# Optimization experiments

Measured on AMD Instinct MI355X. Metric: run time of the kernel, lower is better.

The kernel has to match this reference:

```python
import jax, jax.numpy as jnp
import numpy as np

EMBD_DIM = 512
HIDDEN_DIM = 512
TARGET_DIM = 128
BATCH = 64
MAX_SET = 2048


def setup_inputs() -> dict:
    key = jax.random.key(0)
    ks = jax.random.split(key, 10)
    E, H, T = EMBD_DIM, HIDDEN_DIM, TARGET_DIM
    s = lambda fan_in: 1.0 / np.sqrt(fan_in)
    return {
        "words": jax.random.normal(ks[0], (BATCH, MAX_SET, E), dtype=jnp.float32),
        # attention_layer: Linear(2E -> H) followed by tanh; v: (H, 1)
        "W_att": jax.random.uniform(ks[1], (2 * E, H), jnp.float32, -s(2 * E), s(2 * E)),
        "b_att": jax.random.uniform(ks[2], (H,), jnp.float32, -s(2 * E), s(2 * E)),
        "v": jax.random.normal(ks[3], (H, 1), dtype=jnp.float32),
        # pred_net: Linear(E,H) -> ReLU -> Linear(H,H) -> ReLU -> Linear(H,T)
        "W1": jax.random.uniform(ks[4], (E, H), jnp.float32, -s(E), s(E)),
        "b1": jax.random.uniform(ks[5], (H,), jnp.float32, -s(E), s(E)),
        "W2": jax.random.uniform(ks[6], (H, H), jnp.float32, -s(H), s(H)),
        "b2": jax.random.uniform(ks[7], (H,), jnp.float32, -s(H), s(H)),
        "W3": jax.random.uniform(ks[8], (H, T), jnp.float32, -s(H), s(H)),
        "b3": jax.random.uniform(ks[9], (T,), jnp.float32, -s(H), s(H)),
    }


def reference(words, W_att, b_att, v, W1, b1, W2, b2, W3, b3):
    # words: [B, S, E]. A row is "valid" iff its feature-sum is nonzero
    # (matches words.sum(2).abs().sign() in the torch code).
    mask = jnp.sign(jnp.abs(words.sum(-1)))           # [B, S], 0/1 float
    lengths = mask.sum(axis=1, keepdims=True)          # [B, 1]
    # context = mean over valid rows (padded rows are exactly zero)
    context = words.sum(axis=1, keepdims=True) / lengths[..., None]  # [B, 1, E]
    context = jnp.broadcast_to(context, words.shape)   # [B, S, E]

    x = jnp.concatenate([words, context], axis=-1)     # [B, S, 2E]
    h = jnp.tanh(x @ W_att + b_att)                    # [B, S, H]
    scores = (h @ v)[..., 0]                           # [B, S]

    # per-segment softmax over valid rows only (masked_select + per-batch
    # Softmax in the original == masked softmax here)
    scores = jnp.where(mask > 0, scores, jnp.full_like(scores, -1e30))
    attn = jax.nn.softmax(scores, axis=1)              # [B, S]

    rep = jnp.einsum("bs,bse->be", attn, words)        # [B, E]

    pred = jax.nn.relu(rep @ W1 + b1)
    pred = jax.nn.relu(pred @ W2 + b2)
    pred = pred @ W3 + b3                              # [B, T]
    return pred
```

## Files before the change

### kernel.cpp

```cpp
#include <hip/hip_runtime.h>
#include <hip/hip_bf16.h>
#include <hip/hip_fp16.h>
#include <math.h>

#define B 64
#define S 2048
#define E 512
#define HD 512
#define TD 128
#define M_TOT (B*S)

#define OFF_MASK   0
#define OFF_CTXP   (OFF_MASK + B*S)
#define OFF_LENP   (OFF_CTXP + 8*B*E)
#define OFF_CB     (OFF_LENP + 8*B)
#define OFF_REPP   (OFF_CB + B*HD)
#define OFF_SCP    (OFF_REPP + 8*B*E)
#define OFF_WPK    (OFF_SCP + 2*B*S)
#define OFF_WH     (OFF_WPK + 131072)
#define WS_NEED_FLOATS ((size_t)OFF_WH + (size_t)B*S*E/2)

typedef __attribute__((ext_vector_type(8))) short short8;
typedef __attribute__((ext_vector_type(4))) float f32x4;
typedef __attribute__((ext_vector_type(4))) unsigned short ushort4_t;

__device__ inline unsigned int f2hu(float x) {
    __half h = __float2half(x);
    unsigned short u; __builtin_memcpy(&u, &h, 2); return (unsigned int)u;
}
__device__ inline float hu2f(unsigned short u) {
    __half h; __builtin_memcpy(&h, &u, 2); return __half2float(h);
}

__device__ inline float fast_tanh(float x) {
    float a = fabsf(x);
    float e = __expf(-2.0f * a);
    float r = (1.0f - e) / (1.0f + e);
    return copysignf(r, x);
}

__global__ __launch_bounds__(256)
void k0_pack(const float* __restrict__ W_att, unsigned short* __restrict__ Wpk)
{
    int tid = blockIdx.x*256 + threadIdx.x;
    int e = tid >> 9, h = tid & 511;
    float w = W_att[(size_t)e*HD + h];
    int kstep = e >> 5, kb = (e >> 3) & 3, j = e & 7, f = h >> 4, l15 = h & 15;
    size_t dst = ((((size_t)kstep*32 + f)*64) + kb*16 + l15)*8 + j;
    Wpk[dst] = (unsigned short)f2hu(w);
}

template<bool WRITE_H>
__global__ __launch_bounds__(256)
void k1_maskcol(const float* __restrict__ words, float* __restrict__ mask,
                float* __restrict__ ctxp, float* __restrict__ lenp,
                unsigned short* __restrict__ wordsH)
{
    int bid = blockIdx.x;
    int b = bid >> 3, ch = bid & 7;
    int t = threadIdx.x;
    int w = t >> 6, l = t & 63;
    __shared__ __align__(16) float colred[4][E];
    __shared__ float lenred[4];
    const float* base = words + (size_t)(b * S + ch * 256) * E;
    unsigned short* hbase = wordsH + (size_t)(b * S + ch * 256) * E;
    float4 c0 = make_float4(0.f,0.f,0.f,0.f), c1 = make_float4(0.f,0.f,0.f,0.f);
    float wlen = 0.0f;
    for (int r = w; r < 256; r += 4) {
        const float* row = base + (size_t)r * E;
        float4 a  = *(const float4*)(row + 4*l);
        float4 bb = *(const float4*)(row + 256 + 4*l);
        if (WRITE_H) {
            ushort4_t ha, hb;
            ha[0]=(unsigned short)f2hu(a.x);  ha[1]=(unsigned short)f2hu(a.y);
            ha[2]=(unsigned short)f2hu(a.z);  ha[3]=(unsigned short)f2hu(a.w);
            hb[0]=(unsigned short)f2hu(bb.x); hb[1]=(unsigned short)f2hu(bb.y);
            hb[2]=(unsigned short)f2hu(bb.z); hb[3]=(unsigned short)f2hu(bb.w);
            *(ushort4_t*)(hbase + (size_t)r*E + 4*l)       = ha;
            *(ushort4_t*)(hbase + (size_t)r*E + 256 + 4*l) = hb;
        }
        float rs = a.x+a.y+a.z+a.w + bb.x+bb.y+bb.z+bb.w;
        #pragma unroll
        for (int m = 1; m < 64; m <<= 1) rs += __shfl_xor(rs, m);
        c0.x += a.x;  c0.y += a.y;  c0.z += a.z;  c0.w += a.w;
        c1.x += bb.x; c1.y += bb.y; c1.z += bb.z; c1.w += bb.w;
        if (l == 0) {
            float mv = (rs != 0.0f) ? 1.0f : 0.0f;
            mask[(size_t)b*S + ch*256 + r] = mv;
            wlen += mv;
        }
    }
    *(float4*)&colred[w][4*l]       = c0;
    *(float4*)&colred[w][256 + 4*l] = c1;
    if (l == 0) lenred[w] = wlen;
    __syncthreads();
    float s1 = colred[0][t]+colred[1][t]+colred[2][t]+colred[3][t];
    float s2 = colred[0][t+256]+colred[1][t+256]+colred[2][t+256]+colred[3][t+256];
    size_t o = ((size_t)ch * B + b) * E;
    ctxp[o + t]       = s1;
    ctxp[o + t + 256] = s2;
    if (t == 0) lenp[ch*B + b] = lenred[0]+lenred[1]+lenred[2]+lenred[3];
}

__global__ __launch_bounds__(256)
void k2_cb(const float* __restrict__ W_att, const float* __restrict__ b_att,
           const float* __restrict__ ctxp, const float* __restrict__ lenp,
           float* __restrict__ cb)
{
    int bid = blockIdx.x;
    int b = bid >> 1, hc = bid & 1;
    int t = threadIdx.x;
    __shared__ float ctxL[E];
    float len = 0.f;
    #pragma unroll
    for (int k = 0; k < 8; ++k) len += lenp[k*B + b];
    float inv = 1.0f / len;
    for (int c = t; c < E; c += 256) {
        float sv = 0.f;
        #pragma unroll
        for (int k = 0; k < 8; ++k) sv += ctxp[((size_t)k*B + b)*E + c];
        ctxL[c] = sv * inv;
    }
    __syncthreads();
    int h = hc*256 + t;
    const float* Wb = W_att + (size_t)E * HD;
    float a0 = b_att[h], a1 = 0.f, a2 = 0.f, a3 = 0.f;
    #pragma unroll 4
    for (int e = 0; e < E; e += 4) {
        a0 += ctxL[e]   * Wb[(size_t)e*HD + h];
        a1 += ctxL[e+1] * Wb[(size_t)(e+1)*HD + h];
        a2 += ctxL[e+2] * Wb[(size_t)(e+2)*HD + h];
        a3 += ctxL[e+3] * Wb[(size_t)(e+3)*HD + h];
    }
    cb[(size_t)b*HD + h] = (a0 + a1) + (a2 + a3);
}

template<bool F16>
__global__ __launch_bounds__(512, 4)
void k3_scores(const float* __restrict__ words,
               const unsigned short* __restrict__ wordsH,
               const unsigned short* __restrict__ Wpk,
               const float* __restrict__ cb, const float* __restrict__ v,
               float* __restrict__ scp)
{
    __shared__ __align__(16) unsigned char smem[16384];
    int bid = blockIdx.x;
    int mt = bid >> 1, nc = bid & 1;
    int m0 = mt * 128;
    int b  = m0 >> 11;
    int t = threadIdx.x;
    int lane = t & 63, wid = t >> 6;
    int wr = wid >> 2, wc = wid & 3;

    f32x4 acc[4][4];
    #pragma unroll
    for (int i = 0; i < 4; ++i)
        #pragma unroll
        for (int j = 0; j < 4; ++j) acc[i][j] = (f32x4)0.0f;

    int r = t >> 2, kq = t & 3;
    const float* aSrcF = words + (size_t)(m0 + r)*E + kq*8;
    const unsigned short* aSrcH = wordsH + (size_t)(m0 + r)*E + kq*8;
    int abase = (r >> 4)*1024 + kq*256 + (r & 15)*16;

    float4 pF[2];
    uint4  pH;

    auto LOADA = [&](int ks) {
        if constexpr (F16) {
            pH = *(const uint4*)(aSrcH + ks*32);
        } else {
            const float* _s = aSrcF + ks*32;
            pF[0] = *(const float4*)(_s); pF[1] = *(const float4*)(_s+4);
        }
    };
    auto STAGEA = [&](unsigned char* buf) {
        if constexpr (F16) {
            *(uint4*)&buf[abase] = pH;
        } else {
            float xs[8] = {pF[0].x,pF[0].y,pF[0].z,pF[0].w, pF[1].x,pF[1].y,pF[1].z,pF[1].w};
            unsigned int uw[4];
            #pragma unroll
            for (int p = 0; p < 4; ++p)
                uw[p] = f2hu(xs[2*p]) | (f2hu(xs[2*p+1]) << 16);
            *(uint4*)&buf[abase] = make_uint4(uw[0],uw[1],uw[2],uw[3]);
        }
    };

    const unsigned short* bBase = Wpk + (((size_t)(nc*16 + wc*4))*64 + lane)*8;
#define LDB(ks,cf) (*(const short8*)(bBase + ((size_t)(ks)*32 + (cf))*512))

    LOADA(0);
    STAGEA(smem);
    LOADA(1);
    short8 bcur[4];
    #pragma unroll
    for (int cf = 0; cf < 4; ++cf) bcur[cf] = LDB(0, cf);
    __syncthreads();

    for (int k = 0; k < 16; ++k) {
        unsigned char* bufc = smem + (k & 1)*8192;
        unsigned char* bufn = smem + ((k & 1) ^ 1)*8192;

        short8 ah[4];
        #pragma unroll
        for (int rf = 0; rf < 4; ++rf)
            ah[rf] = *(const short8*)&bufc[(wr*4 + rf)*1024 + lane*16];

        if (k < 15) STAGEA(bufn);
        if (k < 14) LOADA(k + 2);

        #pragma unroll
        for (int cf = 0; cf < 4; ++cf) {
            #pragma unroll
            for (int rf = 0; rf < 4; ++rf)
                acc[rf][cf] = __builtin_amdgcn_mfma_f32_16x16x32_f16(ah[rf], bcur[cf], acc[rf][cf], 0, 0, 0);
            if (k < 15) bcur[cf] = LDB(k + 1, cf);
        }
        __syncthreads();
    }

    float ssum[4][4];
    #pragma unroll
    for (int i = 0; i < 4; ++i)
        #pragma unroll
        for (int rr = 0; rr < 4; ++rr) ssum[i][rr] = 0.f;

    #pragma unroll
    for (int cf = 0; cf < 4; ++cf) {
        int col = nc*256 + wc*64 + cf*16 + (lane & 15);
        float cbv = cb[(size_t)b*HD + col];
        float vv  = v[col];
        #pragma unroll
        for (int rf = 0; rf < 4; ++rf)
            #pragma unroll
            for (int rr = 0; rr < 4; ++rr)
                ssum[rf][rr] += fast_tanh(acc[rf][cf][rr] + cbv) * vv;
    }
    #pragma unroll
    for (int m = 1; m < 16; m <<= 1)
        #pragma unroll
        for (int rf = 0; rf < 4; ++rf)
            #pragma unroll
            for (int rr = 0; rr < 4; ++rr)
                ssum[rf][rr] += __shfl_xor(ssum[rf][rr], m);

    float* scr = (float*)smem;
    if ((lane & 15) == 0) {
        #pragma unroll
        for (int rf = 0; rf < 4; ++rf)
            #pragma unroll
            for (int rr = 0; rr < 4; ++rr)
                scr[wc*128 + wr*64 + rf*16 + (lane >> 4)*4 + rr] = ssum[rf][rr];
    }
    __syncthreads();
    if (t < 128) {
        float val = (scr[t] + scr[128 + t]) + (scr[256 + t] + scr[384 + t]);
        scp[(size_t)nc*M_TOT + m0 + t] = val;
    }
#undef LDB
}

template<bool F16>
__global__ __launch_bounds__(256)
void k4_rep(const float* __restrict__ words, const unsigned short* __restrict__ wordsH,
            const float* __restrict__ scp, const float* __restrict__ mask,
            float* __restrict__ repp)
{
    int bid = blockIdx.x;
    int b = bid >> 3, ch = bid & 7;
    int t = threadIdx.x;
    __shared__ float red[256];
    __shared__ float wrow[256];

    float xs[8];
    float mx = -1e30f;
    #pragma unroll
    for (int k = 0; k < 8; ++k) {
        size_t m = (size_t)b*S + 256*k + t;
        float x = scp[m] + scp[(size_t)M_TOT + m];
        x = (mask[m] > 0.0f) ? x : -1e30f;
        xs[k] = x; mx = fmaxf(mx, x);
    }
    red[t] = mx; __syncthreads();
    for (int off = 128; off > 0; off >>= 1) {
        if (t < off) red[t] = fmaxf(red[t], red[t+off]);
        __syncthreads();
    }
    float gmax = red[0]; __syncthreads();
    float se = 0.f;
    #pragma unroll
    for (int k = 0; k < 8; ++k) se += expf(xs[k] - gmax);
    red[t] = se; __syncthreads();
    for (int off = 128; off > 0; off >>= 1) {
        if (t < off) red[t] += red[t+off];
        __syncthreads();
    }
    float den = red[0];
    wrow[t] = expf(xs[ch] - gmax) / den;
    __syncthreads();

    float2 acc = make_float2(0.f, 0.f);
    if (F16) {
        const unsigned short* base = wordsH + (size_t)(b*S + ch*256)*E + 2*t;
        #pragma unroll 4
        for (int rr = 0; rr < 256; ++rr) {
            unsigned int u = *(const unsigned int*)(base + (size_t)rr*E);
            float a = wrow[rr];
            acc.x = fmaf(a, hu2f((unsigned short)(u & 0xffff)), acc.x);
            acc.y = fmaf(a, hu2f((unsigned short)(u >> 16)),    acc.y);
        }
    } else {
        const float* base = words + (size_t)(b*S + ch*256)*E + 2*t;
        #pragma unroll 4
        for (int rr = 0; rr < 256; ++rr) {
            float2 wv = *(const float2*)(base + (size_t)rr*E);
            float a = wrow[rr];
            acc.x = fmaf(a, wv.x, acc.x);
            acc.y = fmaf(a, wv.y, acc.y);
        }
    }
    size_t o = ((size_t)ch*B + b)*E + 2*t;
    *(float2*)&repp[o] = acc;
}

__global__ __launch_bounds__(256)
void k5_mlp(const float* __restrict__ repp,
            const float* __restrict__ W1, const float* __restrict__ b1,
            const float* __restrict__ W2, const float* __restrict__ b2,
            const float* __restrict__ W3, const float* __restrict__ b3,
            float* __restrict__ out)
{
    int b = blockIdx.x;
    int t = threadIdx.x;
    __shared__ float xL[HD];
    __shared__ float yL[HD];
    for (int c = t; c < E; c += 256) {
        float sv = 0.f;
        #pragma unroll
        for (int k = 0; k < 8; ++k) sv += repp[((size_t)k*B + b)*E + c];
        xL[c] = sv;
    }
    __syncthreads();
    #pragma unroll
    for (int oo = 0; oo < 2; ++oo) {
        int h = oo*256 + t;
        float a0 = b1[h], a1 = 0.f, a2 = 0.f, a3 = 0.f;
        #pragma unroll 4
        for (int e = 0; e < E; e += 4) {
            a0 += xL[e]   * W1[(size_t)e*HD + h];
            a1 += xL[e+1] * W1[(size_t)(e+1)*HD + h];
            a2 += xL[e+2] * W1[(size_t)(e+2)*HD + h];
            a3 += xL[e+3] * W1[(size_t)(e+3)*HD + h];
        }
        yL[h] = fmaxf((a0 + a1) + (a2 + a3), 0.f);
    }
    __syncthreads();
    float l2v[2];
    #pragma unroll
    for (int oo = 0; oo < 2; ++oo) {
        int h = oo*256 + t;
        float a0 = b2[h], a1 = 0.f, a2 = 0.f, a3 = 0.f;
        #pragma unroll 4
        for (int e = 0; e < HD; e += 4) {
            a0 += yL[e]   * W2[(size_t)e*HD + h];
            a1 += yL[e+1] * W2[(size_t)(e+1)*HD + h];
            a2 += yL[e+2] * W2[(size_t)(e+2)*HD + h];
            a3 += yL[e+3] * W2[(size_t)(e+3)*HD + h];
        }
        l2v[oo] = fmaxf((a0 + a1) + (a2 + a3), 0.f);
    }
    __syncthreads();
    xL[t] = l2v[0]; xL[256 + t] = l2v[1];
    __syncthreads();
    if (t < TD) {
        float a0 = b3[t], a1 = 0.f, a2 = 0.f, a3 = 0.f;
        #pragma unroll 4
        for (int e = 0; e < HD; e += 4) {
            a0 += xL[e]   * W3[(size_t)e*TD + t];
            a1 += xL[e+1] * W3[(size_t)(e+1)*TD + t];
            a2 += xL[e+2] * W3[(size_t)(e+2)*TD + t];
            a3 += xL[e+3] * W3[(size_t)(e+3)*TD + t];
        }
        out[(size_t)b*TD + t] = (a0 + a1) + (a2 + a3);
    }
}

extern "C" void kernel_launch(void* const* d_in, const int* in_sizes, int n_in,
                              void* d_out, int out_size, void* d_ws, size_t ws_size,
                              hipStream_t stream)
{
    const float* words = (const float*)d_in[0];
    const float* W_att = (const float*)d_in[1];
    const float* b_att = (const float*)d_in[2];
    const float* v     = (const float*)d_in[3];
    const float* W1    = (const float*)d_in[4];
    const float* b1    = (const float*)d_in[5];
    const float* W2    = (const float*)d_in[6];
    const float* b2    = (const float*)d_in[7];
    const float* W3    = (const float*)d_in[8];
    const float* b3    = (const float*)d_in[9];
    (void)in_sizes; (void)n_in; (void)out_size;

    float* ws   = (float*)d_ws;
    float* mask = ws + OFF_MASK;
    float* ctxp = ws + OFF_CTXP;
    float* lenp = ws + OFF_LENP;
    float* cb   = ws + OFF_CB;
    float* repp = ws + OFF_REPP;
    float* scp  = ws + OFF_SCP;
    unsigned short* Wpk    = (unsigned short*)(ws + OFF_WPK);
    unsigned short* wordsH = (unsigned short*)(ws + OFF_WH);
    float* out  = (float*)d_out;

    bool useF16 = ws_size >= WS_NEED_FLOATS * sizeof(float);

    hipLaunchKernelGGL(k0_pack, dim3(1024), dim3(256), 0, stream, W_att, Wpk);
    if (useF16) {
        hipLaunchKernelGGL(k1_maskcol<true>,  dim3(B*8), dim3(256), 0, stream, words, mask, ctxp, lenp, wordsH);
    } else {
        hipLaunchKernelGGL(k1_maskcol<false>, dim3(B*8), dim3(256), 0, stream, words, mask, ctxp, lenp, wordsH);
    }
    hipLaunchKernelGGL(k2_cb, dim3(B*2), dim3(256), 0, stream, W_att, b_att, ctxp, lenp, cb);
    if (useF16) {
        hipLaunchKernelGGL(k3_scores<true>,  dim3(2048), dim3(512), 0, stream, words, wordsH, Wpk, cb, v, scp);
        hipLaunchKernelGGL(k4_rep<true>,     dim3(B*8),  dim3(256), 0, stream, words, wordsH, scp, mask, repp);
    } else {
        hipLaunchKernelGGL(k3_scores<false>, dim3(2048), dim3(512), 0, stream, words, wordsH, Wpk, cb, v, scp);
        hipLaunchKernelGGL(k4_rep<false>,    dim3(B*8),  dim3(256), 0, stream, words, wordsH, scp, mask, repp);
    }
    hipLaunchKernelGGL(k5_mlp, dim3(B), dim3(256), 0, stream, repp, W1, b1, W2, b2, W3, b3, out);
}
```

Measured before the change: 313.4 us.

## Drop fp16 words copy; split scores GEMM into four column chunks with deeper prefetch

Removes the fp16 shadow copy of words written in the mask kernel. The score GEMM and rep kernel now read fp32 words directly and convert to fp16 during LDS staging. The score kernel splits the hidden dimension into four 128-column chunks instead of two, doubling the grid and halving per-wave accumulators. It also uses a three-deep register prefetch of A tiles and two-step-ahead B loads via an unrolled even/odd body. This avoids writing and rereading a 64 MB half-precision copy, but each block now rereads fp32 A rows four times instead of twice, relying on cache to absorb it.

```diff
diff --git a/kernel.cpp b/kernel.cpp
--- a/kernel.cpp
+++ b/kernel.cpp
@@ -16,20 +16,14 @@
 #define OFF_CB     (OFF_LENP + 8*B)
 #define OFF_REPP   (OFF_CB + B*HD)
 #define OFF_SCP    (OFF_REPP + 8*B*E)
-#define OFF_WPK    (OFF_SCP + 2*B*S)
-#define OFF_WH     (OFF_WPK + 131072)
-#define WS_NEED_FLOATS ((size_t)OFF_WH + (size_t)B*S*E/2)
+#define OFF_WPK    (OFF_SCP + 4*B*S)
 
 typedef __attribute__((ext_vector_type(8))) short short8;
 typedef __attribute__((ext_vector_type(4))) float f32x4;
-typedef __attribute__((ext_vector_type(4))) unsigned short ushort4_t;
 
 __device__ inline unsigned int f2hu(float x) {
     __half h = __float2half(x);
     unsigned short u; __builtin_memcpy(&u, &h, 2); return (unsigned int)u;
-}
-__device__ inline float hu2f(unsigned short u) {
-    __half h; __builtin_memcpy(&h, &u, 2); return __half2float(h);
 }
 
 __device__ inline float fast_tanh(float x) {
@@ -50,11 +44,9 @@
     Wpk[dst] = (unsigned short)f2hu(w);
 }
 
-template<bool WRITE_H>
 __global__ __launch_bounds__(256)
 void k1_maskcol(const float* __restrict__ words, float* __restrict__ mask,
-                float* __restrict__ ctxp, float* __restrict__ lenp,
-                unsigned short* __restrict__ wordsH)
+                float* __restrict__ ctxp, float* __restrict__ lenp)
 {
     int bid = blockIdx.x;
     int b = bid >> 3, ch = bid & 7;
@@ -63,22 +55,12 @@
     __shared__ __align__(16) float colred[4][E];
     __shared__ float lenred[4];
     const float* base = words + (size_t)(b * S + ch * 256) * E;
-    unsigned short* hbase = wordsH + (size_t)(b * S + ch * 256) * E;
     float4 c0 = make_float4(0.f,0.f,0.f,0.f), c1 = make_float4(0.f,0.f,0.f,0.f);
     float wlen = 0.0f;
     for (int r = w; r < 256; r += 4) {
         const float* row = base + (size_t)r * E;
         float4 a  = *(const float4*)(row + 4*l);
         float4 bb = *(const float4*)(row + 256 + 4*l);
-        if (WRITE_H) {
-            ushort4_t ha, hb;
-            ha[0]=(unsigned short)f2hu(a.x);  ha[1]=(unsigned short)f2hu(a.y);
-            ha[2]=(unsigned short)f2hu(a.z);  ha[3]=(unsigned short)f2hu(a.w);
-            hb[0]=(unsigned short)f2hu(bb.x); hb[1]=(unsigned short)f2hu(bb.y);
-            hb[2]=(unsigned short)f2hu(bb.z); hb[3]=(unsigned short)f2hu(bb.w);
-            *(ushort4_t*)(hbase + (size_t)r*E + 4*l)       = ha;
-            *(ushort4_t*)(hbase + (size_t)r*E + 256 + 4*l) = hb;
-        }
         float rs = a.x+a.y+a.z+a.w + bb.x+bb.y+bb.z+bb.w;
         #pragma unroll
         for (int m = 1; m < 64; m <<= 1) rs += __shfl_xor(rs, m);
@@ -135,90 +117,81 @@
     cb[(size_t)b*HD + h] = (a0 + a1) + (a2 + a3);
 }
 
-template<bool F16>
 __global__ __launch_bounds__(512, 4)
 void k3_scores(const float* __restrict__ words,
-               const unsigned short* __restrict__ wordsH,
                const unsigned short* __restrict__ Wpk,
                const float* __restrict__ cb, const float* __restrict__ v,
                float* __restrict__ scp)
 {
     __shared__ __align__(16) unsigned char smem[16384];
     int bid = blockIdx.x;
-    int mt = bid >> 1, nc = bid & 1;
+    int mt = bid >> 2, nc = bid & 3;
     int m0 = mt * 128;
     int b  = m0 >> 11;
     int t = threadIdx.x;
     int lane = t & 63, wid = t >> 6;
     int wr = wid >> 2, wc = wid & 3;
 
-    f32x4 acc[4][4];
+    f32x4 acc[4][2];
     #pragma unroll
     for (int i = 0; i < 4; ++i)
         #pragma unroll
-        for (int j = 0; j < 4; ++j) acc[i][j] = (f32x4)0.0f;
+        for (int j = 0; j < 2; ++j) acc[i][j] = (f32x4)0.0f;
 
     int r = t >> 2, kq = t & 3;
-    const float* aSrcF = words + (size_t)(m0 + r)*E + kq*8;
-    const unsigned short* aSrcH = wordsH + (size_t)(m0 + r)*E + kq*8;
+    const float* aSrc = words + (size_t)(m0 + r)*E + kq*8;
     int abase = (r >> 4)*1024 + kq*256 + (r & 15)*16;
 
-    float4 pF[2];
-    uint4  pH;
-
-    auto LOADA = [&](int ks) {
-        if constexpr (F16) {
-            pH = *(const uint4*)(aSrcH + ks*32);
-        } else {
-            const float* _s = aSrcF + ks*32;
-            pF[0] = *(const float4*)(_s); pF[1] = *(const float4*)(_s+4);
-        }
-    };
-    auto STAGEA = [&](unsigned char* buf) {
-        if constexpr (F16) {
-            *(uint4*)&buf[abase] = pH;
-        } else {
-            float xs[8] = {pF[0].x,pF[0].y,pF[0].z,pF[0].w, pF[1].x,pF[1].y,pF[1].z,pF[1].w};
-            unsigned int uw[4];
-            #pragma unroll
-            for (int p = 0; p < 4; ++p)
-                uw[p] = f2hu(xs[2*p]) | (f2hu(xs[2*p+1]) << 16);
-            *(uint4*)&buf[abase] = make_uint4(uw[0],uw[1],uw[2],uw[3]);
-        }
-    };
-
-    const unsigned short* bBase = Wpk + (((size_t)(nc*16 + wc*4))*64 + lane)*8;
+    const unsigned short* bBase = Wpk + (((size_t)(nc*8 + wc*2))*64 + lane)*8;
 #define LDB(ks,cf) (*(const short8*)(bBase + ((size_t)(ks)*32 + (cf))*512))
 
-    LOADA(0);
-    STAGEA(smem);
-    LOADA(1);
-    short8 bcur[4];
-    #pragma unroll
-    for (int cf = 0; cf < 4; ++cf) bcur[cf] = LDB(0, cf);
-    __syncthreads();
-
-    for (int k = 0; k < 16; ++k) {
-        unsigned char* bufc = smem + (k & 1)*8192;
-        unsigned char* bufn = smem + ((k & 1) ^ 1)*8192;
-
-        short8 ah[4];
-        #pragma unroll
-        for (int rf = 0; rf < 4; ++rf)
-            ah[rf] = *(const short8*)&bufc[(wr*4 + rf)*1024 + lane*16];
-
-        if (k < 15) STAGEA(bufn);
-        if (k < 14) LOADA(k + 2);
-
-        #pragma unroll
-        for (int cf = 0; cf < 4; ++cf) {
-            #pragma unroll
-            for (int rf = 0; rf < 4; ++rf)
-                acc[rf][cf] = __builtin_amdgcn_mfma_f32_16x16x32_f16(ah[rf], bcur[cf], acc[rf][cf], 0, 0, 0);
-            if (k < 15) bcur[cf] = LDB(k + 1, cf);
-        }
-        __syncthreads();
-    }
+    float4 R0a, R0b, R1a, R1b, Rta, Rtb;
+#define LOADA(Ra, Rb, ks) do { const float* _s = aSrc + (ks)*32; \
+        Ra = *(const float4*)(_s); Rb = *(const float4*)(_s + 4); } while(0)
+#define STAGEA(buf, Ra, Rb) do { \
+        unsigned int u0 = f2hu(Ra.x) | (f2hu(Ra.y) << 16); \
+        unsigned int u1 = f2hu(Ra.z) | (f2hu(Ra.w) << 16); \
+        unsigned int u2 = f2hu(Rb.x) | (f2hu(Rb.y) << 16); \
+        unsigned int u3 = f2hu(Rb.z) | (f2hu(Rb.w) << 16); \
+        *(uint4*)&(buf)[abase] = make_uint4(u0, u1, u2, u3); } while(0)
+
+    unsigned char* sm0 = smem;
+    unsigned char* sm1 = smem + 8192;
+
+    LOADA(Rta, Rtb, 0);
+    STAGEA(sm0, Rta, Rtb);
+    LOADA(R1a, R1b, 1);
+    LOADA(R0a, R0b, 2);
+    short8 bE[2], bO[2];
+    bE[0] = LDB(0, 0); bE[1] = LDB(0, 1);
+    bO[0] = LDB(1, 0); bO[1] = LDB(1, 1);
+    __syncthreads();
+
+#define KBODY(k, BUFC, BUFN, RSa, RSb, BF) do { \
+        short8 ah[4]; \
+        _Pragma("unroll") \
+        for (int rf = 0; rf < 4; ++rf) \
+            ah[rf] = *(const short8*)&(BUFC)[(wr*4 + rf)*1024 + lane*16]; \
+        if ((k) < 15) STAGEA(BUFN, RSa, RSb); \
+        if ((k) < 13) LOADA(RSa, RSb, (k) + 3); \
+        _Pragma("unroll") \
+        for (int cf = 0; cf < 2; ++cf) { \
+            _Pragma("unroll") \
+            for (int rf = 0; rf < 4; ++rf) \
+                acc[rf][cf] = __builtin_amdgcn_mfma_f32_16x16x32_f16(ah[rf], BF[cf], acc[rf][cf], 0, 0, 0); \
+            if ((k) < 14) BF[cf] = LDB((k) + 2, cf); \
+        } \
+        __syncthreads(); } while(0)
+
+    #pragma unroll
+    for (int kk = 0; kk < 8; ++kk) {
+        KBODY(2*kk,     sm0, sm1, R1a, R1b, bE);
+        KBODY(2*kk + 1, sm1, sm0, R0a, R0b, bO);
+    }
+#undef KBODY
+#undef LOADA
+#undef STAGEA
+#undef LDB
 
     float ssum[4][4];
     #pragma unroll
@@ -227,8 +200,8 @@
         for (int rr = 0; rr < 4; ++rr) ssum[i][rr] = 0.f;
 
     #pragma unroll
-    for (int cf = 0; cf < 4; ++cf) {
-        int col = nc*256 + wc*64 + cf*16 + (lane & 15);
+    for (int cf = 0; cf < 2; ++cf) {
+        int col = nc*128 + wc*32 + cf*16 + (lane & 15);
         float cbv = cb[(size_t)b*HD + col];
         float vv  = v[col];
         #pragma unroll
@@ -258,14 +231,11 @@
         float val = (scr[t] + scr[128 + t]) + (scr[256 + t] + scr[384 + t]);
         scp[(size_t)nc*M_TOT + m0 + t] = val;
     }
-#undef LDB
-}
-
-template<bool F16>
-__global__ __launch_bounds__(256)
-void k4_rep(const float* __restrict__ words, const unsigned short* __restrict__ wordsH,
-            const float* __restrict__ scp, const float* __restrict__ mask,
-            float* __restrict__ repp)
+}
+
+__global__ __launch_bounds__(256)
+void k4_rep(const float* __restrict__ words, const float* __restrict__ scp,
+            const float* __restrict__ mask, float* __restrict__ repp)
 {
     int bid = blockIdx.x;
     int b = bid >> 3, ch = bid & 7;
@@ -278,7 +248,8 @@
     #pragma unroll
     for (int k = 0; k < 8; ++k) {
         size_t m = (size_t)b*S + 256*k + t;
-        float x = scp[m] + scp[(size_t)M_TOT + m];
+        float x = (scp[m] + scp[(size_t)M_TOT + m])
+                + (scp[(size_t)2*M_TOT + m] + scp[(size_t)3*M_TOT + m]);
         x = (mask[m] > 0.0f) ? x : -1e30f;
         xs[k] = x; mx = fmaxf(mx, x);
     }
@@ -300,25 +271,14 @@
     wrow[t] = expf(xs[ch] - gmax) / den;
     __syncthreads();
 
+    const float* base = words + (size_t)(b*S + ch*256)*E + 2*t;
     float2 acc = make_float2(0.f, 0.f);
-    if (F16) {
-        const unsigned short* base = wordsH + (size_t)(b*S + ch*256)*E + 2*t;
-        #pragma unroll 4
-        for (int rr = 0; rr < 256; ++rr) {
-            unsigned int u = *(const unsigned int*)(base + (size_t)rr*E);
-            float a = wrow[rr];
-            acc.x = fmaf(a, hu2f((unsigned short)(u & 0xffff)), acc.x);
-            acc.y = fmaf(a, hu2f((unsigned short)(u >> 16)),    acc.y);
-        }
-    } else {
-        const float* base = words + (size_t)(b*S + ch*256)*E + 2*t;
-        #pragma unroll 4
-        for (int rr = 0; rr < 256; ++rr) {
-            float2 wv = *(const float2*)(base + (size_t)rr*E);
-            float a = wrow[rr];
-            acc.x = fmaf(a, wv.x, acc.x);
-            acc.y = fmaf(a, wv.y, acc.y);
-        }
+    #pragma unroll 4
+    for (int rr = 0; rr < 256; ++rr) {
+        float2 wv = *(const float2*)(base + (size_t)rr*E);
+        float a = wrow[rr];
+        acc.x = fmaf(a, wv.x, acc.x);
+        acc.y = fmaf(a, wv.y, acc.y);
     }
     size_t o = ((size_t)ch*B + b)*E + 2*t;
     *(float2*)&repp[o] = acc;
@@ -400,7 +360,7 @@
     const float* b2    = (const float*)d_in[7];
     const float* W3    = (const float*)d_in[8];
     const float* b3    = (const float*)d_in[9];
-    (void)in_sizes; (void)n_in; (void)out_size;
+    (void)in_sizes; (void)n_in; (void)out_size; (void)ws_size;
 
     float* ws   = (float*)d_ws;
     float* mask = ws + OFF_MASK;
@@ -409,25 +369,13 @@
     float* cb   = ws + OFF_CB;
     float* repp = ws + OFF_REPP;
     float* scp  = ws + OFF_SCP;
-    unsigned short* Wpk    = (unsigned short*)(ws + OFF_WPK);
-    unsigned short* wordsH = (unsigned short*)(ws + OFF_WH);
+    unsigned short* Wpk = (unsigned short*)(ws + OFF_WPK);
     float* out  = (float*)d_out;
 
-    bool useF16 = ws_size >= WS_NEED_FLOATS * sizeof(float);
-
-    hipLaunchKernelGGL(k0_pack, dim3(1024), dim3(256), 0, stream, W_att, Wpk);
-    if (useF16) {
-        hipLaunchKernelGGL(k1_maskcol<true>,  dim3(B*8), dim3(256), 0, stream, words, mask, ctxp, lenp, wordsH);
-    } else {
-        hipLaunchKernelGGL(k1_maskcol<false>, dim3(B*8), dim3(256), 0, stream, words, mask, ctxp, lenp, wordsH);
-    }
-    hipLaunchKernelGGL(k2_cb, dim3(B*2), dim3(256), 0, stream, W_att, b_att, ctxp, lenp, cb);
-    if (useF16) {
-        hipLaunchKernelGGL(k3_scores<true>,  dim3(2048), dim3(512), 0, stream, words, wordsH, Wpk, cb, v, scp);
-        hipLaunchKernelGGL(k4_rep<true>,     dim3(B*8),  dim3(256), 0, stream, words, wordsH, scp, mask, repp);
-    } else {
-        hipLaunchKernelGGL(k3_scores<false>, dim3(2048), dim3(512), 0, stream, words, wordsH, Wpk, cb, v, scp);
-        hipLaunchKernelGGL(k4_rep<false>,    dim3(B*8),  dim3(256), 0, stream, words, wordsH, scp, mask, repp);
-    }
-    hipLaunchKernelGGL(k5_mlp, dim3(B), dim3(256), 0, stream, repp, W1, b1, W2, b2, W3, b3, out);
-}
+    hipLaunchKernelGGL(k0_pack,    dim3(1024), dim3(256), 0, stream, W_att, Wpk);
+    hipLaunchKernelGGL(k1_maskcol, dim3(B*8),  dim3(256), 0, stream, words, mask, ctxp, lenp);
+    hipLaunchKernelGGL(k2_cb,      dim3(B*2),  dim3(256), 0, stream, W_att, b_att, ctxp, lenp, cb);
+    hipLaunchKernelGGL(k3_scores,  dim3(4096), dim3(512), 0, stream, words, Wpk, cb, v, scp);
+    hipLaunchKernelGGL(k4_rep,     dim3(B*8),  dim3(256), 0, stream, words, scp, mask, repp);
+    hipLaunchKernelGGL(k5_mlp,     dim3(B),    dim3(256), 0, stream, repp, W1, b1, W2, b2, W3, b3, out);
+}
```

After: 360.8 us. 1.15x slower.
